# Performance work log

Measured on AMD Instinct MI355X. Metric: run time of the kernel, lower is better.

## Reference

```python
import jax, jax.numpy as jnp
import numpy as np

B, L, C = 8, 2048, 256
D = C // 8  # qk head dim = 32


def _attn(q, k, v, scale):
    # q:[B,L,D] k:[B,L,D] v:[B,L,Dv] -> [B,L,Dv]
    scores = jnp.einsum('bld,bmd->blm', q, k) / scale
    w = jax.nn.softmax(scores, axis=-1)
    return jnp.einsum('blm,bmd->bld', w, v)


def setup_inputs() -> dict:
    key = jax.random.key(0)
    ks = jax.random.split(key, 16)
    he = lambda k, cin, cout: jax.random.normal(k, (cin, cout), jnp.float32) * np.sqrt(2.0 / cin)
    inp = {'x': jax.random.normal(ks[0], (B, L, C, 2), jnp.float32)}
    # 12 1x1 conv kernels (no bias): Q/K -> C//8, V -> C, for 4 attention blocks
    dims = [D, D, C, D, D, C, D, D, C, D, D, C]
    for i, dout in enumerate(dims):
        inp[f'w{i+1}'] = he(ks[i + 1], C, dout)
    inp['alpha'] = jnp.zeros((1,), jnp.float32)
    inp['gamma'] = jnp.zeros((1,), jnp.float32)
    return inp


def reference(x, w1, w2, w3, w4, w5, w6, w7, w8, w9, w10, w11, w12, alpha, gamma):
    ecg = x[:, :, :, 0]  # [B,L,C]
    pcg = x[:, :, :, 1]
    proj = lambda f, w: jnp.einsum('blc,cd->bld', f, w)  # 1x1 conv, no bias
    scale = jnp.sqrt(jnp.asarray(D, x.dtype))

    # ECG intra-attention
    qkv_ecg_intra = _attn(proj(ecg, w1), proj(ecg, w2), proj(ecg, w3), scale)
    # ECG inter-attention (Q from ECG, K/V from PCG)
    qkv_ecg_inter = _attn(proj(ecg, w4), proj(pcg, w5), proj(pcg, w6), scale)
    ecg_out = qkv_ecg_inter + alpha * qkv_ecg_intra

    # PCG intra-attention
    qkv_pcg_intra = _attn(proj(pcg, w7), proj(pcg, w8), proj(pcg, w9), scale)
    # PCG inter-attention (Q from PCG, K/V from ECG)
    qkv_pcg_inter = _attn(proj(pcg, w10), proj(ecg, w11), proj(ecg, w12), scale)
    pcg_out = qkv_pcg_inter + gamma * qkv_pcg_intra

    return jnp.concatenate([ecg_out, pcg_out], axis=-1)  # [B,L,2C]
```

## Files before the change

kernel.cpp:

```cpp
#include <hip/hip_runtime.h>


typedef __bf16 v8bf __attribute__((ext_vector_type(8)));
typedef float  v16f __attribute__((ext_vector_type(16)));
typedef unsigned int u32;

typedef __attribute__((address_space(1))) const void gvoid;
typedef __attribute__((address_space(3))) void svoid;

#define QSCALE 0.25500526817276613f

union frag_u { u32 d[4]; v8bf v; };
union pk_u { unsigned short s[2]; u32 d; };

static __device__ inline u32 pack_bf16(float x, float y) {
  pk_u u;
  __bf16 a = (__bf16)x, b = (__bf16)y;
  u.s[0] = *(unsigned short*)&a;
  u.s[1] = *(unsigned short*)&b;
  return u.d;
}

__global__ __launch_bounds__(256) void deint_kernel(const float* __restrict__ x,
                                                    __bf16* __restrict__ xe,
                                                    __bf16* __restrict__ xp) {
  const size_t i = (size_t)blockIdx.x * 256 + threadIdx.x;
  const float4* xin = (const float4*)(x + i * 16);
  float4 a = xin[0], b = xin[1], c = xin[2], d = xin[3];
  v8bf ev, pv;
  ev[0]=(__bf16)a.x; ev[1]=(__bf16)a.z; ev[2]=(__bf16)b.x; ev[3]=(__bf16)b.z;
  ev[4]=(__bf16)c.x; ev[5]=(__bf16)c.z; ev[6]=(__bf16)d.x; ev[7]=(__bf16)d.z;
  pv[0]=(__bf16)a.y; pv[1]=(__bf16)a.w; pv[2]=(__bf16)b.y; pv[3]=(__bf16)b.w;
  pv[4]=(__bf16)c.y; pv[5]=(__bf16)c.w; pv[6]=(__bf16)d.y; pv[7]=(__bf16)d.w;
  *(v8bf*)(xe + i * 8) = ev;
  *(v8bf*)(xp + i * 8) = pv;
}

struct ProjArgs {
  const __bf16* xe;
  const __bf16* xp;
  const float* w[12];
  __bf16* q[4];
  __bf16* k[4];
  __bf16* vt[4];
  const float* alpha;
  const float* gamma;
};

__global__ __launch_bounds__(256) void proj_kernel(ProjArgs pa) {
  const int job = blockIdx.x;
  const int rb  = blockIdx.y * 128;
  const int tid = threadIdx.x;
  const int lane = tid & 63, w = tid >> 6;
  const int l31 = lane & 31, lh = lane >> 5;
  const int l7 = lane & 7, l8 = lane >> 3;

  if (job >= 4) {
    const int vi = (job - 4) >> 2;
    if (vi == 0 && pa.alpha[0] == 0.0f) return;
    if (vi == 3 && pa.gamma[0] == 0.0f) return;
  }

  __shared__ __bf16 lds_b[64][264];
  __shared__ __bf16 lds_a[2][128 * 64];

  int src, dout, wc0[2], vcol0 = 0, vmode = 0;
  const float* wp[2];
  __bf16* dqk[2] = {nullptr, nullptr};
  __bf16* vdst = nullptr;
  float sc = 1.0f;
  if (job < 4) {
    dout = 32; wc0[0] = 0; wc0[1] = 0;
    switch (job) {
      case 0: src=0; wp[0]=pa.w[0]; wp[1]=pa.w[3];  dqk[0]=pa.q[0]; dqk[1]=pa.q[1]; sc=QSCALE; break;
      case 1: src=0; wp[0]=pa.w[1]; wp[1]=pa.w[10]; dqk[0]=pa.k[0]; dqk[1]=pa.k[3]; break;
      case 2: src=1; wp[0]=pa.w[6]; wp[1]=pa.w[9];  dqk[0]=pa.q[2]; dqk[1]=pa.q[3]; sc=QSCALE; break;
      default:src=1; wp[0]=pa.w[4]; wp[1]=pa.w[7];  dqk[0]=pa.k[1]; dqk[1]=pa.k[2]; break;
    }
  } else {
    const int vi = (job - 4) >> 2, t = (job - 4) & 3;
    const int widx = (vi==0) ? 2 : (vi==1) ? 11 : (vi==2) ? 5 : 8;
    const int vbuf = (vi==0) ? 0 : (vi==1) ? 3  : (vi==2) ? 1 : 2;
    dout = 256; vmode = 1; src = vi >> 1;
    wp[0] = pa.w[widx]; wp[1] = pa.w[widx];
    wc0[0] = t*64; wc0[1] = t*64 + 32;
    vcol0 = t*64; vdst = pa.vt[vbuf];
  }

  for (int h = 0; h < 2; ++h) {
    const float* wgt = wp[h]; const int c0 = wc0[h];
    for (int i = tid; i < 32*256; i += 256) {
      int n = i & 31, kk = i >> 5;
      lds_b[h*32 + n][kk] = (__bf16)wgt[(size_t)kk*dout + c0 + n];
    }
  }

  const __bf16* X = src ? pa.xp : pa.xe;
  const char* agbase = (const char*)(X + (size_t)rb*256) + (size_t)(l7 ^ l8)*16
                     + (size_t)l8*512;

#define STAGE_A(buf, kb)                                                        \
  {                                                                             \
    const char* g = agbase + (size_t)(kb)*128;                                  \
    _Pragma("unroll")                                                           \
    for (int i = 0; i < 4; ++i)                                                 \
      __builtin_amdgcn_global_load_lds(                                         \
          (gvoid*)(g + (size_t)(w*4 + i)*8*512),                                \
          (svoid*)&lds_a[buf][((w*4 + i)*8)*64 + lane*8], 16, 0, 0);            \
  }

  STAGE_A(0, 0)
  __syncthreads();

  v16f acc[2];
#pragma unroll
  for (int n = 0; n < 2; ++n)
#pragma unroll
    for (int i = 0; i < 16; ++i) acc[n][i] = 0.f;

  for (int kb = 0; kb < 4; ++kb) {
    if (kb < 3) STAGE_A((kb + 1) & 1, kb + 1)
    const __bf16* ab = &lds_a[kb & 1][0];
#pragma unroll
    for (int kk = 0; kk < 4; ++kk) {
      const v8bf af = *(const v8bf*)&ab[(w*32 + l31)*64 + (((kk*2 + lh) ^ (l31 & 7))*8)];
#pragma unroll
      for (int nt = 0; nt < 2; ++nt) {
        const v8bf bf = *(const v8bf*)&lds_b[nt*32 + l31][kb*64 + kk*16 + lh*8];
        acc[nt] = __builtin_amdgcn_mfma_f32_32x32x16_bf16(af, bf, acc[nt], 0, 0, 0);
      }
    }
    __syncthreads();
  }

  if (!vmode) {
#pragma unroll
    for (int nt = 0; nt < 2; ++nt) {
      __bf16* dst = dqk[nt];
#pragma unroll
      for (int r = 0; r < 16; ++r) {
        const int row = rb + w*32 + (r & 3) + 8*(r >> 2) + 4*lh;
        dst[(size_t)row*32 + l31] = (__bf16)(acc[nt][r] * sc);
      }
    }
  } else {
    __bf16 (*lds_t)[136] = (__bf16 (*)[136])&lds_a[0][0];
#pragma unroll
    for (int nt = 0; nt < 2; ++nt) {
#pragma unroll
      for (int r = 0; r < 16; ++r) {
        const int row = w*32 + (r & 3) + 8*(r >> 2) + 4*lh;
        lds_t[nt*32 + l31][row] = (__bf16)acc[nt][r];
      }
    }
    __syncthreads();
    const int bb = rb >> 11, ll0 = rb & 2047;
    const int nt0 = vcol0 >> 5;
    const size_t tbase = (size_t)(bb*32 + (ll0 >> 6));
    for (int i = tid; i < 1024; i += 256) {
      const int ktl = i >> 9, s = i & 511;
      const int h = s >> 8, kc2 = (s >> 5) & 7, v5 = s & 31;
      const int vrow = h*32 + v5, krow = ktl*64 + kc2*8;
      *(int4*)&vdst[((tbase + ktl)*2048 + (size_t)((nt0 + h)*8 + kc2)*32 + v5) * 8] =
          *(const int4*)&lds_t[vrow][krow];
    }
  }
}

struct FlashArgs {
  const __bf16* q[4];
  const __bf16* k[4];
  const __bf16* v[4];
  const float* alpha;
  const float* gamma;
  float* out;
};

__global__ __launch_bounds__(256, 3) void flash_half(FlashArgs fa) {
  const int flat = blockIdx.x;
  const int pair = flat & 31, qt = flat >> 5;
  const int att = pair & 3, bb = pair >> 2;
  const int tid = threadIdx.x;
  const int lane = tid & 63, w = tid >> 6;
  const int l31 = lane & 31, lh = lane >> 5;

  const float av = fa.alpha[0], gv = fa.gamma[0];
  int att_e, nt0;
  if (att == 0)      { if (av != 0.0f) return; att_e = 1; nt0 = 4; }
  else if (att == 1) { if (av != 0.0f) return; att_e = 1; nt0 = 0; }
  else if (att == 2) { if (gv != 0.0f) return; att_e = 3; nt0 = 4; }
  else               { if (gv != 0.0f) return; att_e = 3; nt0 = 0; }

  __shared__ __bf16 v_lds[2][8192];

  const __bf16* Qp = fa.q[att_e] + (size_t)(bb*2048 + qt*128 + w*32 + l31)*32;
  const __bf16* Kb = fa.k[att_e] + (size_t)bb*2048*32;
  const char* vgbase = (const char*)(fa.v[att_e] + (size_t)bb*32*16384)
                     + (size_t)(nt0*256 + w*256 + lane)*16;
  float* outp = fa.out + (size_t)(bb*2048 + qt*128 + w*32)*512
              + (att_e >> 1)*256 + nt0*32;

  const v8bf qf0 = *(const v8bf*)&Qp[lh*8];
  const v8bf qf1 = *(const v8bf*)&Qp[16 + lh*8];

#define HSTAGE(buf_, kt_)                                                       \
  {                                                                             \
    const char* g = vgbase + (size_t)(kt_)*32768;                               \
    _Pragma("unroll")                                                           \
    for (int i = 0; i < 4; ++i)                                                 \
      __builtin_amdgcn_global_load_lds(                                         \
          (gvoid*)(g + (size_t)i*1024),                                         \
          (svoid*)&v_lds[buf_][(w*256 + 64*i)*8 + lane*8], 16, 0, 0);           \
  }

#define HLOADK(a_, b_, c_, d_, kt_)                                             \
  {                                                                             \
    const int kb_ = (kt_) * 64;                                                 \
    a_ = *(const v8bf*)&Kb[((size_t)(kb_ +      l31))*32 +      lh*8];          \
    b_ = *(const v8bf*)&Kb[((size_t)(kb_ +      l31))*32 + 16 + lh*8];          \
    c_ = *(const v8bf*)&Kb[((size_t)(kb_ + 32 + l31))*32 +      lh*8];          \
    d_ = *(const v8bf*)&Kb[((size_t)(kb_ + 32 + l31))*32 + 16 + lh*8];          \
  }

  v16f acc[4];
#pragma unroll
  for (int n = 0; n < 4; ++n)
#pragma unroll
    for (int i = 0; i < 16; ++i) acc[n][i] = 0.f;
  float den_s = 0.f;

  v8bf kfc00, kfc01, kfc10, kfc11;
  HLOADK(kfc00, kfc01, kfc10, kfc11, 0)
  HSTAGE(0, 0)
  __syncthreads();

#pragma unroll 1
  for (int kt = 0; kt < 32; ++kt) {
    const int cur = kt & 1;
    v8bf kfn00, kfn01, kfn10, kfn11;
    if (kt < 31) {
      HLOADK(kfn00, kfn01, kfn10, kfn11, kt + 1)
      HSTAGE(cur ^ 1, kt + 1)
    }

    v16f st0, st1;
#pragma unroll
    for (int i = 0; i < 16; ++i) { st0[i] = 0.f; st1[i] = 0.f; }
    st0 = __builtin_amdgcn_mfma_f32_32x32x16_bf16(kfc00, qf0, st0, 0, 0, 0);
    st0 = __builtin_amdgcn_mfma_f32_32x32x16_bf16(kfc01, qf1, st0, 0, 0, 0);
    st1 = __builtin_amdgcn_mfma_f32_32x32x16_bf16(kfc10, qf0, st1, 0, 0, 0);
    st1 = __builtin_amdgcn_mfma_f32_32x32x16_bf16(kfc11, qf1, st1, 0, 0, 0);

    u32 pk0[8], pk1[8];
#pragma unroll
    for (int i = 0; i < 8; ++i) {
      const float e0 = __builtin_exp2f(st0[2*i]);
      const float e1 = __builtin_exp2f(st0[2*i + 1]);
      den_s += e0 + e1;
      pk0[i] = pack_bf16(e0, e1);
    }
#pragma unroll
    for (int i = 0; i < 8; ++i) {
      const float e0 = __builtin_exp2f(st1[2*i]);
      const float e1 = __builtin_exp2f(st1[2*i + 1]);
      den_s += e0 + e1;
      pk1[i] = pack_bf16(e0, e1);
    }

    v8bf pf[4];
#pragma unroll
    for (int f2 = 0; f2 < 2; ++f2) {
      u32 a0 = pk0[f2*4 + 0], b0 = pk0[f2*4 + 2];
      u32 a1 = pk0[f2*4 + 1], b1 = pk0[f2*4 + 3];
      asm("v_permlane32_swap_b32 %0, %1" : "+v"(a0), "+v"(b0));
      asm("v_permlane32_swap_b32 %0, %1" : "+v"(a1), "+v"(b1));
      frag_u fu;
      fu.d[0] = a0; fu.d[1] = a1; fu.d[2] = b0; fu.d[3] = b1;
      pf[f2] = fu.v;
    }
#pragma unroll
    for (int f2 = 0; f2 < 2; ++f2) {
      u32 a0 = pk1[f2*4 + 0], b0 = pk1[f2*4 + 2];
      u32 a1 = pk1[f2*4 + 1], b1 = pk1[f2*4 + 3];
      asm("v_permlane32_swap_b32 %0, %1" : "+v"(a0), "+v"(b0));
      asm("v_permlane32_swap_b32 %0, %1" : "+v"(a1), "+v"(b1));
      frag_u fu;
      fu.d[0] = a0; fu.d[1] = a1; fu.d[2] = b0; fu.d[3] = b1;
      pf[2 + f2] = fu.v;
    }

    const __bf16* vb = &v_lds[cur][0];
#pragma unroll
    for (int kc = 0; kc < 4; ++kc)
#pragma unroll
      for (int nt = 0; nt < 4; ++nt) {
        const v8bf vf = *(const v8bf*)&vb[(nt*256 + kc*64 + lane)*8];
        acc[nt] = __builtin_amdgcn_mfma_f32_32x32x16_bf16(pf[kc], vf, acc[nt], 0, 0, 0);
      }

    __syncthreads();
    if (kt < 31) { kfc00 = kfn00; kfc01 = kfn01; kfc10 = kfn10; kfc11 = kfn11; }
  }

  const float den_full = den_s + __shfl_xor(den_s, 32, 64);
#pragma unroll
  for (int r = 0; r < 16; ++r) {
    const int row = (r & 3) + 8*(r >> 2) + 4*lh;
    const float f = 1.0f / __shfl(den_full, row, 64);
#pragma unroll
    for (int nt = 0; nt < 4; ++nt)
      outp[(size_t)row*512 + nt*32 + l31] = acc[nt][r] * f;
  }

#undef HSTAGE
#undef HLOADK
}

template<int NTN>
__device__ __forceinline__ void flash_body(
    const __bf16* __restrict__ Qp, const __bf16* __restrict__ Kb,
    const char* __restrict__ vgbase, float scv, float* __restrict__ outp,
    __bf16* __restrict__ lds0, int lane, int w, int l31, int lh) {

  __bf16* vb0 = lds0;
  __bf16* vb1 = lds0 + NTN*2048;

  const v8bf qf0 = *(const v8bf*)&Qp[lh*8];
  const v8bf qf1 = *(const v8bf*)&Qp[16 + lh*8];

#define STAGE_V(dst_, kt_)                                                      \
  {                                                                             \
    const char* g = vgbase + (size_t)(kt_)*32768;                               \
    _Pragma("unroll")                                                           \
    for (int i = 0; i < NTN; ++i)                                               \
      __builtin_amdgcn_global_load_lds(                                         \
          (gvoid*)(g + (size_t)i*1024),                                         \
          (svoid*)&dst_[(w*NTN*64 + 64*i)*8 + lane*8], 16, 0, 0);               \
  }

  v16f acc[NTN];
#pragma unroll
  for (int n = 0; n < NTN; ++n)
#pragma unroll
    for (int i = 0; i < 16; ++i) acc[n][i] = 0.f;

  float den_s = 0.f;
  v8bf pf[4];
  v8bf kf00, kf01, kf10, kf11;
  v16f st0, st1;
  u32 pk0[8], pk1[8];

#define LOADK(kt_)                                                              \
  {                                                                             \
    const int kb_ = (kt_) * 64;                                                 \
    kf00 = *(const v8bf*)&Kb[((size_t)(kb_ +      l31))*32 +      lh*8];        \
    kf01 = *(const v8bf*)&Kb[((size_t)(kb_ +      l31))*32 + 16 + lh*8];        \
    kf10 = *(const v8bf*)&Kb[((size_t)(kb_ + 32 + l31))*32 +      lh*8];        \
    kf11 = *(const v8bf*)&Kb[((size_t)(kb_ + 32 + l31))*32 + 16 + lh*8];        \
  }

#define SMFMA                                                                   \
  {                                                                             \
    _Pragma("unroll")                                                           \
    for (int i = 0; i < 16; ++i) { st0[i] = 0.f; st1[i] = 0.f; }                \
    st0 = __builtin_amdgcn_mfma_f32_32x32x16_bf16(kf00, qf0, st0, 0, 0, 0);     \
    st0 = __builtin_amdgcn_mfma_f32_32x32x16_bf16(kf01, qf1, st0, 0, 0, 0);     \
    st1 = __builtin_amdgcn_mfma_f32_32x32x16_bf16(kf10, qf0, st1, 0, 0, 0);     \
    st1 = __builtin_amdgcn_mfma_f32_32x32x16_bf16(kf11, qf1, st1, 0, 0, 0);     \
  }

#define EXPH(st_, pk_)                                                          \
  _Pragma("unroll")                                                             \
  for (int i = 0; i < 8; ++i) {                                                 \
    const float e0 = __builtin_exp2f(st_[2*i]);                                 \
    const float e1 = __builtin_exp2f(st_[2*i + 1]);                             \
    den_s += e0 + e1;                                                           \
    pk_[i] = pack_bf16(e0, e1);                                                 \
  }

#define XCHG(pk_, o_)                                                           \
  _Pragma("unroll")                                                             \
  for (int f2 = 0; f2 < 2; ++f2) {                                              \
    u32 a0 = pk_[f2*4 + 0], b0 = pk_[f2*4 + 2];                                 \
    u32 a1 = pk_[f2*4 + 1], b1 = pk_[f2*4 + 3];                                 \
    asm("v_permlane32_swap_b32 %0, %1" : "+v"(a0), "+v"(b0));                   \
    asm("v_permlane32_swap_b32 %0, %1" : "+v"(a1), "+v"(b1));                   \
    frag_u fu;                                                                  \
    fu.d[0] = a0; fu.d[1] = a1; fu.d[2] = b0; fu.d[3] = b1;                     \
    pf[(o_) + f2] = fu.v;                                                       \
  }

#define PVBLK(kc_, vb_)                                                         \
  _Pragma("unroll")                                                             \
  for (int nt = 0; nt < NTN; ++nt) {                                            \
    const v8bf vf = *(const v8bf*)&vb_[(nt*256 + (kc_)*64 + lane)*8];           \
    acc[nt] = __builtin_amdgcn_mfma_f32_32x32x16_bf16(pf[kc_], vf, acc[nt], 0, 0, 0); \
  }

  LOADK(0)
  STAGE_V(vb0, 0)
  SMFMA
  EXPH(st0, pk0)
  EXPH(st1, pk1)
  XCHG(pk0, 0)
  XCHG(pk1, 2)
  __syncthreads();

  for (int kt = 0; kt < 31; ++kt) {
    const int cur = kt & 1;
    LOADK(kt + 1)
    if (cur) { STAGE_V(vb0, kt + 1) } else { STAGE_V(vb1, kt + 1) }
    const __bf16* vb = cur ? vb1 : vb0;

    PVBLK(0, vb)
    SMFMA
    PVBLK(1, vb)
    EXPH(st0, pk0)
    PVBLK(2, vb)
    EXPH(st1, pk1)
    XCHG(pk0, 0)
    PVBLK(3, vb)
    XCHG(pk1, 2)

    __syncthreads();
  }

  {
    PVBLK(0, vb1)
    PVBLK(1, vb1)
    PVBLK(2, vb1)
    PVBLK(3, vb1)
  }

  const float den_full = den_s + __shfl_xor(den_s, 32, 64);
#pragma unroll
  for (int r = 0; r < 16; ++r) {
    const int row = (r & 3) + 8*(r >> 2) + 4*lh;
    const float f = scv / __shfl(den_full, row, 64);
#pragma unroll
    for (int nt = 0; nt < NTN; ++nt)
      unsafeAtomicAdd(&outp[(size_t)row*512 + nt*32 + l31], acc[nt][r] * f);
  }

#undef STAGE_V
#undef LOADK
#undef SMFMA
#undef EXPH
#undef XCHG
#undef PVBLK
}

__global__ __launch_bounds__(256, 2) void flash_full(FlashArgs fa) {
  const int flat = blockIdx.x;
  const int pair = flat & 31, qt = flat >> 5;
  const int att = pair & 3, bb = pair >> 2;
  const int tid = threadIdx.x;
  const int lane = tid & 63, w = tid >> 6;
  const int l31 = lane & 31, lh = lane >> 5;

  const float av = fa.alpha[0], gv = fa.gamma[0];
  float scv = 1.0f;
  if (att == 0)      { if (av == 0.0f) return; scv = av; }
  else if (att == 1) { if (av == 0.0f) return; }
  else if (att == 2) { if (gv == 0.0f) return; scv = gv; }
  else               { if (gv == 0.0f) return; }

  __shared__ __bf16 v_lds[2][16384];

  const __bf16* Qp = fa.q[att] + (size_t)(bb*2048 + qt*128 + w*32 + l31)*32;
  const __bf16* Kb = fa.k[att] + (size_t)bb*2048*32;
  const char* vgbase = (const char*)(fa.v[att] + (size_t)bb*32*16384)
                     + (size_t)(w*512 + lane)*16;
  float* outp = fa.out + (size_t)(bb*2048 + qt*128 + w*32)*512 + (att >> 1)*256;

  flash_body<8>(Qp, Kb, vgbase, scv, outp, &v_lds[0][0], lane, w, l31, lh);
}

extern "C" void kernel_launch(void* const* d_in, const int* in_sizes, int n_in,
                              void* d_out, int out_size, void* d_ws, size_t ws_size,
                              hipStream_t stream) {
  (void)in_sizes; (void)n_in; (void)out_size; (void)ws_size;

  __bf16* wsp = (__bf16*)d_ws;
  const size_t XE = (size_t)16384 * 256;
  const size_t QK = (size_t)16384 * 32;
  const size_t VT = (size_t)8 * 32 * 16384;

  __bf16* xe = wsp;
  __bf16* xp = wsp + XE;

  ProjArgs pa;
  pa.xe = xe; pa.xp = xp;
  const float* x = (const float*)d_in[0];
  for (int i = 0; i < 12; ++i) pa.w[i] = (const float*)d_in[1 + i];
  __bf16* base = wsp + 2*XE;
  for (int i = 0; i < 4; ++i) pa.q[i]  = base + (size_t)i * QK;
  for (int i = 0; i < 4; ++i) pa.k[i]  = base + (size_t)(4 + i) * QK;
  for (int i = 0; i < 4; ++i) pa.vt[i] = base + 8*QK + (size_t)i * VT;
  pa.alpha = (const float*)d_in[13];
  pa.gamma = (const float*)d_in[14];

  hipMemsetAsync(d_out, 0, (size_t)8*2048*512*4, stream);
  hipLaunchKernelGGL(deint_kernel, dim3(2048), dim3(256), 0, stream, x, xe, xp);
  hipLaunchKernelGGL(proj_kernel, dim3(20, 128), dim3(256), 0, stream, pa);

  FlashArgs fl;
  for (int i = 0; i < 4; ++i) { fl.q[i] = pa.q[i]; fl.k[i] = pa.k[i]; fl.v[i] = pa.vt[i]; }
  fl.alpha = (const float*)d_in[13];
  fl.gamma = (const float*)d_in[14];
  fl.out = (float*)d_out;
  hipLaunchKernelGGL(flash_half, dim3(512), dim3(256), 0, stream, fl);
  hipLaunchKernelGGL(flash_full, dim3(512), dim3(256), 0, stream, fl);
}
```

Measured before the change: 230.8 us.

## Merge projection jobs per source so each block reuses staged input tile

The projection kernel now launches one block per source signal and row tile instead of one per output job. Each block stages its full 128x256 input tile into LDS once and loops over up to ten weight chunks (Q, K and the V column tiles), so the input is no longer reloaded for every job. The cost is a grid that shrinks from 2560 to 256 blocks, which lowers parallelism on a GPU with many CUs, serializes the per-chunk weight loads inside each block, and adds more LDS per block.

New measurement: 246.8 us. 1.07x slower.

```diff
diff --git a/kernel.cpp b/kernel.cpp
--- a/kernel.cpp
+++ b/kernel.cpp
@@ -55,116 +55,118 @@
   const int l31 = lane & 31, lh = lane >> 5;
   const int l7 = lane & 7, l8 = lane >> 3;
 
-  if (job >= 4) {
-    const int vi = (job - 4) >> 2;
-    if (vi == 0 && pa.alpha[0] == 0.0f) return;
-    if (vi == 3 && pa.gamma[0] == 0.0f) return;
-  }
-
+  __shared__ __bf16 lds_a[4][128 * 64];
   __shared__ __bf16 lds_b[64][264];
-  __shared__ __bf16 lds_a[2][128 * 64];
-
-  int src, dout, wc0[2], vcol0 = 0, vmode = 0;
-  const float* wp[2];
-  __bf16* dqk[2] = {nullptr, nullptr};
-  __bf16* vdst = nullptr;
-  float sc = 1.0f;
-  if (job < 4) {
-    dout = 32; wc0[0] = 0; wc0[1] = 0;
-    switch (job) {
-      case 0: src=0; wp[0]=pa.w[0]; wp[1]=pa.w[3];  dqk[0]=pa.q[0]; dqk[1]=pa.q[1]; sc=QSCALE; break;
-      case 1: src=0; wp[0]=pa.w[1]; wp[1]=pa.w[10]; dqk[0]=pa.k[0]; dqk[1]=pa.k[3]; break;
-      case 2: src=1; wp[0]=pa.w[6]; wp[1]=pa.w[9];  dqk[0]=pa.q[2]; dqk[1]=pa.q[3]; sc=QSCALE; break;
-      default:src=1; wp[0]=pa.w[4]; wp[1]=pa.w[7];  dqk[0]=pa.k[1]; dqk[1]=pa.k[2]; break;
-    }
-  } else {
-    const int vi = (job - 4) >> 2, t = (job - 4) & 3;
-    const int widx = (vi==0) ? 2 : (vi==1) ? 11 : (vi==2) ? 5 : 8;
-    const int vbuf = (vi==0) ? 0 : (vi==1) ? 3  : (vi==2) ? 1 : 2;
-    dout = 256; vmode = 1; src = vi >> 1;
-    wp[0] = pa.w[widx]; wp[1] = pa.w[widx];
-    wc0[0] = t*64; wc0[1] = t*64 + 32;
-    vcol0 = t*64; vdst = pa.vt[vbuf];
-  }
-
-  for (int h = 0; h < 2; ++h) {
-    const float* wgt = wp[h]; const int c0 = wc0[h];
-    for (int i = tid; i < 32*256; i += 256) {
-      int n = i & 31, kk = i >> 5;
-      lds_b[h*32 + n][kk] = (__bf16)wgt[(size_t)kk*dout + c0 + n];
-    }
-  }
-
-  const __bf16* X = src ? pa.xp : pa.xe;
+  __shared__ __bf16 lds_t[64][136];
+
+  const float gate = job ? pa.gamma[0] : pa.alpha[0];
+  const int nchunks = (gate != 0.0f) ? 10 : 6;
+
+  const __bf16* X = job ? pa.xp : pa.xe;
   const char* agbase = (const char*)(X + (size_t)rb*256) + (size_t)(l7 ^ l8)*16
                      + (size_t)l8*512;
 
-#define STAGE_A(buf, kb)                                                        \
+#define STAGE_A(kb)                                                             \
   {                                                                             \
     const char* g = agbase + (size_t)(kb)*128;                                  \
     _Pragma("unroll")                                                           \
     for (int i = 0; i < 4; ++i)                                                 \
       __builtin_amdgcn_global_load_lds(                                         \
           (gvoid*)(g + (size_t)(w*4 + i)*8*512),                                \
-          (svoid*)&lds_a[buf][((w*4 + i)*8)*64 + lane*8], 16, 0, 0);            \
-  }
-
-  STAGE_A(0, 0)
+          (svoid*)&lds_a[kb][((w*4 + i)*8)*64 + lane*8], 16, 0, 0);             \
+  }
+
+  STAGE_A(0) STAGE_A(1) STAGE_A(2) STAGE_A(3)
   __syncthreads();
 
-  v16f acc[2];
-#pragma unroll
-  for (int n = 0; n < 2; ++n)
-#pragma unroll
-    for (int i = 0; i < 16; ++i) acc[n][i] = 0.f;
-
-  for (int kb = 0; kb < 4; ++kb) {
-    if (kb < 3) STAGE_A((kb + 1) & 1, kb + 1)
-    const __bf16* ab = &lds_a[kb & 1][0];
-#pragma unroll
-    for (int kk = 0; kk < 4; ++kk) {
-      const v8bf af = *(const v8bf*)&ab[(w*32 + l31)*64 + (((kk*2 + lh) ^ (l31 & 7))*8)];
+  const int bb = rb >> 11, ll0 = rb & 2047;
+
+  for (int c = 0; c < nchunks; ++c) {
+    int vmode = 0, dout = 32, wc0[2] = {0, 0}, vcol0 = 0;
+    float sc = 1.0f;
+    const float* wp[2];
+    __bf16* dqk[2] = {nullptr, nullptr};
+    __bf16* vdst = nullptr;
+    if (c == 0) {
+      sc = QSCALE;
+      wp[0] = pa.w[job ? 6 : 0]; wp[1] = pa.w[job ? 9 : 3];
+      dqk[0] = pa.q[job ? 2 : 0]; dqk[1] = pa.q[job ? 3 : 1];
+    } else if (c == 1) {
+      wp[0] = pa.w[job ? 4 : 1]; wp[1] = pa.w[job ? 7 : 10];
+      dqk[0] = pa.k[job ? 1 : 0]; dqk[1] = pa.k[job ? 2 : 3];
+    } else {
+      vmode = 1; dout = 256;
+      const int t = (c - 2) & 3;
+      const bool second = (c >= 6);
+      const int widx = job ? (second ? 8 : 5) : (second ? 2 : 11);
+      const int vbuf = job ? (second ? 2 : 1) : (second ? 0 : 3);
+      wp[0] = pa.w[widx]; wp[1] = pa.w[widx];
+      wc0[0] = t*64; wc0[1] = t*64 + 32;
+      vcol0 = t*64; vdst = pa.vt[vbuf];
+    }
+
+    for (int h = 0; h < 2; ++h) {
+      const float* wgt = wp[h]; const int c0 = wc0[h];
+      for (int i = tid; i < 32*256; i += 256) {
+        int n = i & 31, kk = i >> 5;
+        lds_b[h*32 + n][kk] = (__bf16)wgt[(size_t)kk*dout + c0 + n];
+      }
+    }
+    __syncthreads();
+
+    v16f acc[2];
+#pragma unroll
+    for (int n = 0; n < 2; ++n)
+#pragma unroll
+      for (int i = 0; i < 16; ++i) acc[n][i] = 0.f;
+
+#pragma unroll
+    for (int kb = 0; kb < 4; ++kb) {
+      const __bf16* ab = &lds_a[kb][0];
+#pragma unroll
+      for (int kk = 0; kk < 4; ++kk) {
+        const v8bf af = *(const v8bf*)&ab[(w*32 + l31)*64 + (((kk*2 + lh) ^ (l31 & 7))*8)];
+#pragma unroll
+        for (int nt = 0; nt < 2; ++nt) {
+          const v8bf bf = *(const v8bf*)&lds_b[nt*32 + l31][kb*64 + kk*16 + lh*8];
+          acc[nt] = __builtin_amdgcn_mfma_f32_32x32x16_bf16(af, bf, acc[nt], 0, 0, 0);
+        }
+      }
+    }
+    __syncthreads();
+
+    if (!vmode) {
 #pragma unroll
       for (int nt = 0; nt < 2; ++nt) {
-        const v8bf bf = *(const v8bf*)&lds_b[nt*32 + l31][kb*64 + kk*16 + lh*8];
-        acc[nt] = __builtin_amdgcn_mfma_f32_32x32x16_bf16(af, bf, acc[nt], 0, 0, 0);
+        __bf16* dst = dqk[nt];
+#pragma unroll
+        for (int r = 0; r < 16; ++r) {
+          const int row = rb + w*32 + (r & 3) + 8*(r >> 2) + 4*lh;
+          dst[(size_t)row*32 + l31] = (__bf16)(acc[nt][r] * sc);
+        }
       }
-    }
-    __syncthreads();
-  }
-
-  if (!vmode) {
-#pragma unroll
-    for (int nt = 0; nt < 2; ++nt) {
-      __bf16* dst = dqk[nt];
-#pragma unroll
-      for (int r = 0; r < 16; ++r) {
-        const int row = rb + w*32 + (r & 3) + 8*(r >> 2) + 4*lh;
-        dst[(size_t)row*32 + l31] = (__bf16)(acc[nt][r] * sc);
+    } else {
+#pragma unroll
+      for (int nt = 0; nt < 2; ++nt) {
+#pragma unroll
+        for (int r = 0; r < 16; ++r) {
+          const int row = w*32 + (r & 3) + 8*(r >> 2) + 4*lh;
+          lds_t[nt*32 + l31][row] = (__bf16)acc[nt][r];
+        }
       }
-    }
-  } else {
-    __bf16 (*lds_t)[136] = (__bf16 (*)[136])&lds_a[0][0];
-#pragma unroll
-    for (int nt = 0; nt < 2; ++nt) {
-#pragma unroll
-      for (int r = 0; r < 16; ++r) {
-        const int row = w*32 + (r & 3) + 8*(r >> 2) + 4*lh;
-        lds_t[nt*32 + l31][row] = (__bf16)acc[nt][r];
+      __syncthreads();
+      const int nt0 = vcol0 >> 5;
+      const size_t tbase = (size_t)(bb*32 + (ll0 >> 6));
+      for (int i = tid; i < 1024; i += 256) {
+        const int ktl = i >> 9, s = i & 511;
+        const int h = s >> 8, kc2 = (s >> 5) & 7, v5 = s & 31;
+        const int vrow = h*32 + v5, krow = ktl*64 + kc2*8;
+        *(int4*)&vdst[((tbase + ktl)*2048 + (size_t)((nt0 + h)*8 + kc2)*32 + v5) * 8] =
+            *(const int4*)&lds_t[vrow][krow];
       }
     }
-    __syncthreads();
-    const int bb = rb >> 11, ll0 = rb & 2047;
-    const int nt0 = vcol0 >> 5;
-    const size_t tbase = (size_t)(bb*32 + (ll0 >> 6));
-    for (int i = tid; i < 1024; i += 256) {
-      const int ktl = i >> 9, s = i & 511;
-      const int h = s >> 8, kc2 = (s >> 5) & 7, v5 = s & 31;
-      const int vrow = h*32 + v5, krow = ktl*64 + kc2*8;
-      *(int4*)&vdst[((tbase + ktl)*2048 + (size_t)((nt0 + h)*8 + kc2)*32 + v5) * 8] =
-          *(const int4*)&lds_t[vrow][krow];
-    }
-  }
+  }
+#undef STAGE_A
 }
 
 struct FlashArgs {
@@ -502,7 +504,7 @@
 
   hipMemsetAsync(d_out, 0, (size_t)8*2048*512*4, stream);
   hipLaunchKernelGGL(deint_kernel, dim3(2048), dim3(256), 0, stream, x, xe, xp);
-  hipLaunchKernelGGL(proj_kernel, dim3(20, 128), dim3(256), 0, stream, pa);
+  hipLaunchKernelGGL(proj_kernel, dim3(2, 128), dim3(256), 0, stream, pa);
 
   FlashArgs fl;
   for (int i = 0; i < 4; ++i) { fl.q[i] = pa.q[i]; fl.k[i] = pa.k[i]; fl.v[i] = pa.vt[i]; }
```
